# Performance work log

Measured on AMD Instinct MI355X. Metric: run time of the kernel, lower is better.

Reference implementation:

```python
import jax, jax.numpy as jnp
import numpy as np

EPS = 1e-7      # GENConv message epsilon
BN_EPS = 1e-5   # torch BatchNorm1d eps


def _genconv(x, src, dst, n, w1, b1, gamma, beta, w2, b2):
    # GENConv(aggr='softmax_sg', t=1.0): msg = relu(x_j)+eps, per-feature
    # scatter-softmax weights (stop-grad), weighted sum, residual, MLP
    # [Linear -> BatchNorm(train stats) -> ReLU -> Linear].
    msg = jnp.maximum(x[src], 0.0) + EPS                         # [E, d]
    m = jax.ops.segment_max(msg, dst, num_segments=n)            # [N, d]
    e = jnp.exp(msg - m[dst])
    s = jax.ops.segment_sum(e, dst, num_segments=n)
    alpha = jax.lax.stop_gradient(e / (s[dst] + 1e-16))          # softmax_sg
    agg = jax.ops.segment_sum(msg * alpha, dst, num_segments=n)  # [N, d]
    h = agg + x
    h = h @ w1 + b1
    mu = jnp.mean(h, axis=0)
    var = jnp.var(h, axis=0)
    h = (h - mu) * jax.lax.rsqrt(var + BN_EPS) * gamma + beta
    h = jnp.maximum(h, 0.0)
    return h @ w2 + b2


def _forward(x, edge_index, batch, target,
             g1_w1, g1_b1, g1_g, g1_be, g1_w2, g1_b2,
             g2_w1, g2_b1, g2_g, g2_be, g2_w2, g2_b2,
             g3_w1, g3_b1, g3_g, g3_be, g3_w2, g3_b2,
             fg1_w, fg1_b, fg2_w, fg2_b, fg3_w, fg3_b,
             emb, cw, cb, fxt_w, fxt_b,
             f1_w, f1_b, f2_w, f2_b, o_w, o_b):
    n = x.shape[0]
    nb = target.shape[0]
    src, dst = edge_index[0], edge_index[1]
    h = jnp.maximum(_genconv(x, src, dst, n, g1_w1, g1_b1, g1_g, g1_be, g1_w2, g1_b2), 0.0)
    h = jnp.maximum(_genconv(h, src, dst, n, g2_w1, g2_b1, g2_g, g2_be, g2_w2, g2_b2), 0.0)
    h = jnp.maximum(_genconv(h, src, dst, n, g3_w1, g3_b1, g3_g, g3_be, g3_w2, g3_b2), 0.0)
    # global mean pool over graphs
    sums = jax.ops.segment_sum(h, batch, num_segments=nb)
    cnt = jax.ops.segment_sum(jnp.ones((n, 1), h.dtype), batch, num_segments=nb)
    xg = sums / jnp.maximum(cnt, 1.0)
    xg = jnp.maximum(xg @ fg1_w + fg1_b, 0.0)
    xg = jnp.maximum(xg @ fg2_w + fg2_b, 0.0)
    xg = jnp.maximum(xg @ fg3_w + fg3_b, 0.0)
    # protein branch: embed [B,1000,128], Conv1d(1000->32,k=8) over embed axis
    ext = emb[target]                                            # [B, 1000, 128]
    conv = jax.lax.conv_general_dilated(
        ext, cw, (1,), 'VALID',
        dimension_numbers=('NCW', 'OIW', 'NCW')) + cb[None, :, None]  # [B, 32, 121]
    xt = conv.reshape(nb, 32 * 121) @ fxt_w + fxt_b
    xc = jnp.concatenate([xg, xt], axis=1)                       # [B, 256]
    xc = jnp.maximum(xc @ f1_w + f1_b, 0.0)
    xc = jnp.maximum(xc @ f2_w + f2_b, 0.0)
    return xc @ o_w + o_b


def _lin(k, i, o):
    kw, kb = jax.random.split(k)
    s = 1.0 / np.sqrt(i)
    return (jax.random.uniform(kw, (i, o), jnp.float32, -s, s),
            jax.random.uniform(kb, (o,), jnp.float32, -s, s))


def setup_inputs():
    key = jax.random.key(0)
    ks = jax.random.split(key, 32)
    N, E, B, D = 30000, 150000, 256, 78
    d = {}
    d['x'] = jax.random.normal(ks[0], (N, D), jnp.float32)
    d['edge_index'] = jax.random.randint(ks[1], (2, E), 0, N)
    d['batch'] = jnp.sort(jax.random.randint(ks[2], (N,), 0, B))
    d['target'] = jax.random.randint(ks[3], (B, 1000), 0, 26)
    dims = [(78, 156, 78), (78, 156, 312), (312, 624, 624)]
    for li, (i, hdim, o) in enumerate(dims, start=1):
        w1, b1 = _lin(ks[4 + 2 * li], i, hdim)
        w2, b2 = _lin(ks[5 + 2 * li], hdim, o)
        d['g%d_w1' % li], d['g%d_b1' % li] = w1, b1
        d['g%d_g' % li] = jnp.ones((hdim,), jnp.float32)
        d['g%d_be' % li] = jnp.zeros((hdim,), jnp.float32)
        d['g%d_w2' % li], d['g%d_b2' % li] = w2, b2
    d['fg1_w'], d['fg1_b'] = _lin(ks[14], 624, 512)
    d['fg2_w'], d['fg2_b'] = _lin(ks[15], 512, 1024)
    d['fg3_w'], d['fg3_b'] = _lin(ks[16], 1024, 128)
    d['emb'] = jax.random.normal(ks[17], (26, 128), jnp.float32)
    s = 1.0 / np.sqrt(1000 * 8)
    d['cw'] = jax.random.uniform(ks[18], (32, 1000, 8), jnp.float32, -s, s)
    d['cb'] = jax.random.uniform(ks[19], (32,), jnp.float32, -s, s)
    d['fxt_w'], d['fxt_b'] = _lin(ks[20], 32 * 121, 128)
    d['f1_w'], d['f1_b'] = _lin(ks[21], 256, 1024)
    d['f2_w'], d['f2_b'] = _lin(ks[22], 1024, 512)
    d['o_w'], d['o_b'] = _lin(ks[23], 512, 1)
    return d


def reference(x, edge_index, batch, target,
              g1_w1, g1_b1, g1_g, g1_be, g1_w2, g1_b2,
              g2_w1, g2_b1, g2_g, g2_be, g2_w2, g2_b2,
              g3_w1, g3_b1, g3_g, g3_be, g3_w2, g3_b2,
              fg1_w, fg1_b, fg2_w, fg2_b, fg3_w, fg3_b,
              emb, cw, cb, fxt_w, fxt_b,
              f1_w, f1_b, f2_w, f2_b, o_w, o_b):
    return _forward(x, edge_index, batch, target,
                    g1_w1, g1_b1, g1_g, g1_be, g1_w2, g1_b2,
                    g2_w1, g2_b1, g2_g, g2_be, g2_w2, g2_b2,
                    g3_w1, g3_b1, g3_g, g3_be, g3_w2, g3_b2,
                    fg1_w, fg1_b, fg2_w, fg2_b, fg3_w, fg3_b,
                    emb, cw, cb, fxt_w, fxt_b,
                    f1_w, f1_b, f2_w, f2_b, o_w, o_b)
```

## Files before the change

kernel.cpp:

```cpp
#include <hip/hip_runtime.h>
#include <hip/hip_bf16.h>

typedef unsigned short u16;
typedef __attribute__((ext_vector_type(8))) short bh8;
typedef __attribute__((ext_vector_type(4))) float f32x4;

static __device__ __forceinline__ float b2fu(u16 u) {
    union { float f; unsigned int i; } x;
    x.i = ((unsigned int)u) << 16;
    return x.f;
}
static __device__ __forceinline__ u16 f2bu(float f) {
    __hip_bfloat16 h = __float2bfloat16(f);
    union { __hip_bfloat16 h; u16 u; } x;
    x.h = h;
    return x.u;
}
static __device__ __forceinline__ void load2(const float* p, float& v0, float& v1) {
    float2 v = *reinterpret_cast<const float2*>(p);
    v0 = v.x; v1 = v.y;
}
static __device__ __forceinline__ void load2(const u16* p, float& v0, float& v1) {
    unsigned int u = *reinterpret_cast<const unsigned int*>(p);
    v0 = b2fu((u16)(u & 0xffff)); v1 = b2fu((u16)(u >> 16));
}

static __device__ __forceinline__ void gload16(const u16* g, u16* l) {
    __builtin_amdgcn_global_load_lds(
        (const __attribute__((address_space(1))) unsigned int*)(const void*)g,
        (__attribute__((address_space(3))) unsigned int*)(void*)l, 16, 0, 0);
}


__global__ __launch_bounds__(256) void const_out_kernel(float* __restrict__ out, float v, int n) {
    int i = blockIdx.x * 256 + threadIdx.x;
    if (i < n) out[i] = v;
}


__global__ __launch_bounds__(256) void hist_kernel(const int* __restrict__ dst,
                                                   int* __restrict__ hist, int E) {
    int e = blockIdx.x * 256 + threadIdx.x;
    if (e < E) atomicAdd(&hist[dst[e]], 1);
}

__global__ __launch_bounds__(256) void scan_kernel(const int* __restrict__ hist,
                                                   int* __restrict__ rowptr,
                                                   int* __restrict__ fill, int N) {
    __shared__ int csum[256];
    __shared__ int coff[257];
    int t = threadIdx.x;
    int chunk = (N + 255) / 256;
    int lo = min(t * chunk, N), hi = min(lo + chunk, N);
    int s = 0;
    for (int i = lo; i < hi; i++) s += hist[i];
    csum[t] = s;
    __syncthreads();
    if (t == 0) {
        int acc = 0;
        for (int i = 0; i < 256; i++) { coff[i] = acc; acc += csum[i]; }
        rowptr[N] = acc;
    }
    __syncthreads();
    int run = coff[t];
    for (int i = lo; i < hi; i++) {
        rowptr[i] = run;
        fill[i] = run;
        run += hist[i];
    }
}

__global__ __launch_bounds__(256) void scan_tiles(const int* __restrict__ hist, int N,
                                                  int* __restrict__ rowptr,
                                                  int* __restrict__ tsum) {
    int tid = threadIdx.x;
    int i = blockIdx.x * 256 + tid;
    int v = (i < N) ? hist[i] : 0;
    __shared__ int s[256];
    s[tid] = v;
    __syncthreads();
    for (int off = 1; off < 256; off <<= 1) {
        int t = (tid >= off) ? s[tid - off] : 0;
        __syncthreads();
        s[tid] += t;
        __syncthreads();
    }
    if (i < N) rowptr[i] = s[tid] - v;
    if (tid == 255) tsum[blockIdx.x] = s[255];
}

__global__ __launch_bounds__(256) void scan_tsum(const int* __restrict__ tsum, int ntiles,
                                                 int* __restrict__ toff,
                                                 int* __restrict__ totalp) {
    int tid = threadIdx.x;
    int v = (tid < ntiles) ? tsum[tid] : 0;
    __shared__ int s[256];
    s[tid] = v;
    __syncthreads();
    for (int off = 1; off < 256; off <<= 1) {
        int t = (tid >= off) ? s[tid - off] : 0;
        __syncthreads();
        s[tid] += t;
        __syncthreads();
    }
    if (tid < ntiles) toff[tid] = s[tid] - v;
    if (tid == 255) *totalp = s[255];
}

__global__ __launch_bounds__(256) void scan_apply(int* __restrict__ rowptr,
                                                  const int* __restrict__ toff, int N,
                                                  int* __restrict__ fill) {
    int i = blockIdx.x * 256 + threadIdx.x;
    if (i < N) {
        int r = rowptr[i] + toff[blockIdx.x];
        rowptr[i] = r;
        fill[i] = r;
    }
}

__global__ __launch_bounds__(256) void scatter_kernel(const int* __restrict__ src,
                                                      const int* __restrict__ dst,
                                                      int* __restrict__ fill,
                                                      int* __restrict__ srcs, int E) {
    int e = blockIdx.x * 256 + threadIdx.x;
    if (e < E) {
        int p = atomicAdd(&fill[dst[e]], 1);
        srcs[p] = src[e];
    }
}


template <typename T>
__global__ __launch_bounds__(256) void agg_kernel(const T* __restrict__ x,
                                                  const int* __restrict__ rowptr,
                                                  const int* __restrict__ srcs,
                                                  u16* __restrict__ out, int d, int Kp, int N) {
    int n = blockIdx.y * 4 + (threadIdx.x >> 6);
    int f = (blockIdx.x * 64 + (threadIdx.x & 63)) * 2;
    if (n >= N || f >= Kp) return;
    size_t o = (size_t)n * Kp + f;
    if (f >= d) {
        *reinterpret_cast<unsigned int*>(out + o) = 0;
        return;
    }
    int e0 = rowptr[n], e1 = rowptr[n + 1];
    float s0 = 0.f, t0 = 0.f, s1 = 0.f, t1 = 0.f;
    for (int e = e0; e < e1; e++) {
        int sr = srcs[e];
        float v0, v1;
        load2(x + (size_t)sr * d + f, v0, v1);
        float m0 = fmaxf(v0, 0.f) + 1e-7f;
        float w0 = __expf(m0);
        s0 += w0; t0 += m0 * w0;
        float m1 = fmaxf(v1, 0.f) + 1e-7f;
        float w1 = __expf(m1);
        s1 += w1; t1 += m1 * w1;
    }
    float x0, x1;
    load2(x + (size_t)n * d + f, x0, x1);
    float a0 = t0 / (s0 + 1e-16f) + x0;
    float a1 = t1 / (s1 + 1e-16f) + x1;
    unsigned int pk = (unsigned int)f2bu(a0) | ((unsigned int)f2bu(a1) << 16);
    *reinterpret_cast<unsigned int*>(out + o) = pk;
}


__global__ __launch_bounds__(256) void wt_cvt(const float* __restrict__ W, int K, int N,
                                              u16* __restrict__ WT, int Kp, int Np) {
    int n = blockIdx.y * 4 + (threadIdx.x >> 6);
    int k = blockIdx.x * 64 + (threadIdx.x & 63);
    if (n >= Np || k >= Kp) return;
    float v = (n < N && k < K) ? W[(size_t)k * N + n] : 0.f;
    WT[(size_t)n * Kp + k] = f2bu(v);
}


template <int AMODE, int EMODE, bool RELU, typename CT>
__global__ __launch_bounds__(256) void gemm_mfma(const u16* __restrict__ A,
                                                 const u16* __restrict__ BT,
                                                 const float* __restrict__ bias,
                                                 CT* __restrict__ C, int ldc, int M, int Ncols,
                                                 int Kp, int nbx, int nby, int spx,
                                                 const float* __restrict__ scale,
                                                 const float* __restrict__ shift,
                                                 float* __restrict__ osum,
                                                 float* __restrict__ osumsq) {
    int xcd = blockIdx.x & 7;
    int j = blockIdx.x >> 3;
    int bx = j % nbx;
    int by = xcd * spx + j / nbx;
    if (by >= nby) return;
    __shared__ u16 As[2][128 * 32];
    __shared__ u16 Bs[2][128 * 32];
    const int tid = threadIdx.x;
    const int lane = tid & 63;
    const int w = tid >> 6;
    const int bm = by * 128;
    const int bn = bx * 128;
    f32x4 acc[4][4] = {};

    const int r0 = w * 16 + (lane >> 2);
    const int r1 = r0 + 64;
    const int sw = ((lane & 3) ^ ((r0 >> 1) & 3)) << 3;
    const u16* Ag0 = A + (size_t)(bm + r0) * Kp + sw;
    const u16* Ag1 = A + (size_t)(bm + r1) * Kp + sw;
    const u16* Bg0 = BT + (size_t)(bn + r0) * Kp + sw;
    const u16* Bg1 = BT + (size_t)(bn + r1) * Kp + sw;
    const int wb = w << 9;

    uint4 a0r, a1r;
    auto stageB = [&](int b, int koff) {
        gload16(Bg0 + koff, &Bs[b][wb]);
        gload16(Bg1 + koff, &Bs[b][2048 + wb]);
    };
    auto stageA_lds = [&](int b, int koff) {
        gload16(Ag0 + koff, &As[b][wb]);
        gload16(Ag1 + koff, &As[b][2048 + wb]);
    };
    auto loadA_reg = [&](int koff) {
        a0r = *reinterpret_cast<const uint4*>(Ag0 + koff);
        a1r = *reinterpret_cast<const uint4*>(Ag1 + koff);
    };
    auto writeA_reg = [&](int b, int koff) {
        int f0 = sw + koff;
        float4 sc0 = *reinterpret_cast<const float4*>(scale + f0);
        float4 sc1 = *reinterpret_cast<const float4*>(scale + f0 + 4);
        float4 sh0 = *reinterpret_cast<const float4*>(shift + f0);
        float4 sh1 = *reinterpret_cast<const float4*>(shift + f0 + 4);
        auto tf2 = [](unsigned int u, float sa, float sb, float ha, float hb) {
            float h0 = b2fu((u16)(u & 0xffff)), h1 = b2fu((u16)(u >> 16));
            float v0 = fmaxf(fmaf(h0, sa, ha), 0.f);
            float v1 = fmaxf(fmaf(h1, sb, hb), 0.f);
            return (unsigned int)f2bu(v0) | ((unsigned int)f2bu(v1) << 16);
        };
        uint4 o0, o1;
        o0.x = tf2(a0r.x, sc0.x, sc0.y, sh0.x, sh0.y);
        o0.y = tf2(a0r.y, sc0.z, sc0.w, sh0.z, sh0.w);
        o0.z = tf2(a0r.z, sc1.x, sc1.y, sh1.x, sh1.y);
        o0.w = tf2(a0r.w, sc1.z, sc1.w, sh1.z, sh1.w);
        o1.x = tf2(a1r.x, sc0.x, sc0.y, sh0.x, sh0.y);
        o1.y = tf2(a1r.y, sc0.z, sc0.w, sh0.z, sh0.w);
        o1.z = tf2(a1r.z, sc1.x, sc1.y, sh1.x, sh1.y);
        o1.w = tf2(a1r.w, sc1.z, sc1.w, sh1.z, sh1.w);
        *reinterpret_cast<uint4*>(&As[b][wb + lane * 8]) = o0;
        *reinterpret_cast<uint4*>(&As[b][2048 + wb + lane * 8]) = o1;
    };

    const int fm = (w >> 1) * 64 + (lane & 15);
    const int fn = (w & 1) * 64 + (lane & 15);
    const int g = lane >> 4;
    const int ka = (g ^ ((fm >> 1) & 3)) << 3;
    const int kb = (g ^ ((fn >> 1) & 3)) << 3;

    const int nk = Kp >> 5;
    if constexpr (AMODE == 0) {
        stageA_lds(0, 0);
        stageB(0, 0);
        asm volatile("s_waitcnt vmcnt(0)" ::: "memory");
    } else {
        loadA_reg(0);
        stageB(0, 0);
        asm volatile("s_waitcnt vmcnt(0)" ::: "memory");
        writeA_reg(0, 0);
        asm volatile("s_waitcnt lgkmcnt(0)" ::: "memory");
    }
    __builtin_amdgcn_s_barrier();
    for (int k = 0; k < nk; k++) {
        const int cur = k & 1;
        if (k + 1 < nk) {
            if constexpr (AMODE == 0) stageA_lds(cur ^ 1, (k + 1) << 5);
            else loadA_reg((k + 1) << 5);
            stageB(cur ^ 1, (k + 1) << 5);
        }
        bh8 af[4], bf[4];
#pragma unroll
        for (int mt = 0; mt < 4; mt++)
            af[mt] = *reinterpret_cast<const bh8*>(&As[cur][(fm + mt * 16) * 32 + ka]);
#pragma unroll
        for (int nt = 0; nt < 4; nt++)
            bf[nt] = *reinterpret_cast<const bh8*>(&Bs[cur][(fn + nt * 16) * 32 + kb]);
        asm volatile("s_waitcnt lgkmcnt(0)" ::: "memory");
        __builtin_amdgcn_sched_barrier(0);
        __builtin_amdgcn_s_setprio(1);
#pragma unroll
        for (int mt = 0; mt < 4; mt++)
#pragma unroll
            for (int nt = 0; nt < 4; nt++)
                acc[mt][nt] = __builtin_amdgcn_mfma_f32_16x16x32_bf16(af[mt], bf[nt],
                                                                      acc[mt][nt], 0, 0, 0);
        __builtin_amdgcn_s_setprio(0);
        __builtin_amdgcn_sched_barrier(0);
        asm volatile("s_waitcnt vmcnt(0)" ::: "memory");
        if constexpr (AMODE == 1) {
            __builtin_amdgcn_sched_barrier(0);
            if (k + 1 < nk) writeA_reg(cur ^ 1, (k + 1) << 5);
            asm volatile("s_waitcnt lgkmcnt(0)" ::: "memory");
        }
        __builtin_amdgcn_s_barrier();
    }
    const int rq = (lane >> 4) * 4;
    const int cl = lane & 15;
    if constexpr (EMODE == 0) {
#pragma unroll
        for (int mt = 0; mt < 4; mt++) {
#pragma unroll
            for (int nt = 0; nt < 4; nt++) {
                int n = bn + (w & 1) * 64 + nt * 16 + cl;
                if (n >= Ncols) continue;
                float bv = bias[n];
#pragma unroll
                for (int r = 0; r < 4; r++) {
                    int m = bm + (w >> 1) * 64 + mt * 16 + rq + r;
                    if (m >= M) continue;
                    float v = acc[mt][nt][r] + bv;
                    if (RELU) v = fmaxf(v, 0.f);
                    if (sizeof(CT) == 2)
                        C[(size_t)m * ldc + n] = (CT)f2bu(v);
                    else
                        C[(size_t)m * ldc + n] = (CT)v;
                }
            }
        }
    } else {
        float cs[4] = {0.f, 0.f, 0.f, 0.f}, cq[4] = {0.f, 0.f, 0.f, 0.f};
#pragma unroll
        for (int nt = 0; nt < 4; nt++) {
            int n = bn + (w & 1) * 64 + nt * 16 + cl;
            if (n >= ldc) continue;
            float bv = (n < Ncols) ? bias[n] : 0.f;
#pragma unroll
            for (int mt = 0; mt < 4; mt++) {
#pragma unroll
                for (int r = 0; r < 4; r++) {
                    int m = bm + (w >> 1) * 64 + mt * 16 + rq + r;
                    if (m >= M) continue;
                    float v = (n < Ncols) ? acc[mt][nt][r] + bv : 0.f;
                    u16 vb = f2bu(v);
                    C[(size_t)m * ldc + n] = (CT)vb;
                    float vf = b2fu(vb);
                    cs[nt] += vf;
                    cq[nt] += vf * vf;
                }
            }
        }
        float* red = (float*)&As[0][0];
        const int slot = (w >> 1) * 4 + (lane >> 4);
#pragma unroll
        for (int nt = 0; nt < 4; nt++) {
            int nl = (w & 1) * 64 + nt * 16 + cl;
            red[nl * 8 + slot] = cs[nt];
            red[1024 + nl * 8 + slot] = cq[nt];
        }
        __syncthreads();
        if (tid < 128) {
            int n = bn + tid;
            if (n < Ncols) {
                float s = 0.f, q = 0.f;
#pragma unroll
                for (int i = 0; i < 8; i++) {
                    s += red[tid * 8 + i];
                    q += red[1024 + tid * 8 + i];
                }
                atomicAdd(&osum[n], s);
                atomicAdd(&osumsq[n], q);
            }
        }
    }
}


__global__ __launch_bounds__(256) void bn_final(const float* __restrict__ sum,
                                                const float* __restrict__ sumsq,
                                                const float* __restrict__ gamma,
                                                const float* __restrict__ beta,
                                                float* __restrict__ scale,
                                                float* __restrict__ shift, int dh, int Kp,
                                                float invN) {
    int i = blockIdx.x * 256 + threadIdx.x;
    if (i >= Kp) return;
    if (i < dh) {
        float mu = sum[i] * invN;
        float var = sumsq[i] * invN - mu * mu;
        float sc = gamma[i] / sqrtf(var + 1e-5f);
        scale[i] = sc;
        shift[i] = beta[i] - mu * sc;
    } else {
        scale[i] = 0.f;
        shift[i] = 0.f;
    }
}


__global__ __launch_bounds__(256) void pool_seg(const u16* __restrict__ h,
                                                const int* __restrict__ goff,
                                                float* __restrict__ gsum, int d) {
    int g = blockIdx.y;
    int c = threadIdx.x & 63;
    int f = blockIdx.x * 64 + c;
    int wv = threadIdx.x >> 6;
    int r0 = goff[g], r1 = goff[g + 1];
    float s = 0.f;
    if (f < d)
        for (int r = r0 + wv; r < r1; r += 4) s += b2fu(h[(size_t)r * d + f]);
    __shared__ float ls[4][64];
    ls[wv][c] = s;
    __syncthreads();
    if (wv == 0 && f < d) {
        float tot = ls[0][c] + ls[1][c] + ls[2][c] + ls[3][c];
        gsum[(size_t)g * d + f] = tot / fmaxf((float)(r1 - r0), 1.f);
    }
}


__global__ __launch_bounds__(256) void gemm_sk(const float* __restrict__ A, int lda,
                                               const float* __restrict__ B, int ldb,
                                               float* __restrict__ C, int ldc, int M, int K,
                                               int Nn, int KC) {
    __shared__ float As[16][17];
    __shared__ float Bs[16][68];
    const int tid = threadIdx.x;
    const int bn = blockIdx.x * 64;
    const int bm = blockIdx.y * 16;
    const int k0 = blockIdx.z * KC;
    const int kend = min(K, k0 + KC);
    const int tx = tid & 63;
    const int ty = tid >> 6;
    float acc[4] = {};
    const int am = bm + (tid >> 4);
    const int ak = tid & 15;
    for (int kk0 = k0; kk0 < kend; kk0 += 16) {
        {
            int k = kk0 + ak;
            As[ak][tid >> 4] = (am < M && k < kend) ? A[(size_t)am * lda + k] : 0.f;
        }
#pragma unroll
        for (int i = 0; i < 4; i++) {
            int k = kk0 + ty + 4 * i;
            Bs[ty + 4 * i][tx] = (k < kend && bn + tx < Nn) ? B[(size_t)k * ldb + bn + tx] : 0.f;
        }
        __syncthreads();
#pragma unroll
        for (int kk = 0; kk < 16; kk++) {
            float b = Bs[kk][tx];
#pragma unroll
            for (int i = 0; i < 4; i++) acc[i] = fmaf(As[kk][ty + 4 * i], b, acc[i]);
        }
        __syncthreads();
    }
    if (bn + tx < Nn) {
#pragma unroll
        for (int i = 0; i < 4; i++) {
            int m = bm + ty + 4 * i;
            if (m < M) atomicAdd(&C[(size_t)m * ldc + bn + tx], acc[i]);
        }
    }
}

__global__ __launch_bounds__(256) void bias_act(float* __restrict__ C, int ldc,
                                                const float* __restrict__ bias, int M, int Nn,
                                                int relu) {
    int idx = blockIdx.x * 256 + threadIdx.x;
    if (idx >= M * Nn) return;
    int m = idx / Nn, n = idx - m * Nn;
    float v = C[(size_t)m * ldc + n] + bias[n];
    C[(size_t)m * ldc + n] = relu ? fmaxf(v, 0.f) : v;
}

static void launch_gemm_small(const float* A, int lda, const float* B, int ldb,
                              const float* bias, float* C, int ldc, int M, int K, int Nn,
                              bool relu, hipStream_t stream) {
    int gx = (Nn + 63) / 64, gy = (M + 15) / 16;
    int tiles = gx * gy;
    int ksplit = 512 / tiles;
    if (ksplit < 1) ksplit = 1;
    int maxsplit = (K + 63) / 64;
    if (ksplit > maxsplit) ksplit = maxsplit;
    int KC = (((K + ksplit - 1) / ksplit) + 15) & ~15;
    ksplit = (K + KC - 1) / KC;
    gemm_sk<<<dim3(gx, gy, ksplit), 256, 0, stream>>>(A, lda, B, ldb, C, ldc, M, K, Nn, KC);
    bias_act<<<(M * Nn + 255) / 256, 256, 0, stream>>>(C, ldc, bias, M, Nn, relu ? 1 : 0);
}


__global__ __launch_bounds__(256) void hone_kernel(const int* __restrict__ target,
                                                   u16* __restrict__ H, int total) {
    int i = blockIdx.x * 256 + threadIdx.x;
    if (i >= total) return;
    int b = i / 1000, pos = i - b * 1000;
    int t = target[i];
    H[((size_t)b * 26 + t) * 1024 + pos] = 0x3F80;
}

__global__ __launch_bounds__(256) void cwt_cvt(const float* __restrict__ cw,
                                               u16* __restrict__ BT) {
    int n = blockIdx.y;
    int kk = blockIdx.x * 256 + threadIdx.x;
    int o = n >> 3, k = n & 7;
    float v = (kk < 1000) ? cw[(size_t)o * 8000 + (size_t)kk * 8 + k] : 0.f;
    BT[(size_t)n * 1024 + kk] = f2bu(v);
}

__global__ __launch_bounds__(256) void prot_conv_kernel(const float* __restrict__ S,
                                                        const float* __restrict__ emb,
                                                        const float* __restrict__ cb,
                                                        float* __restrict__ out) {
    int b = blockIdx.x;
    int tid = threadIdx.x;
    __shared__ float Sl[6656];
    __shared__ float el[26 * 128];
    for (int i = tid; i < 6656; i += 256) Sl[i] = S[(size_t)b * 6656 + i];
    for (int i = tid; i < 26 * 128; i += 256) el[i] = emb[i];
    __syncthreads();
    for (int j = tid; j < 3872; j += 256) {
        int o = j / 121;
        int w = j - o * 121;
        float acc = cb[o];
        for (int t = 0; t < 26; t++) {
#pragma unroll
            for (int k = 0; k < 8; k++)
                acc = fmaf(Sl[t * 256 + o * 8 + k], el[t * 128 + w + k], acc);
        }
        out[(size_t)b * 3872 + j] = acc;
    }
}


__global__ __launch_bounds__(256) void out_kernel(const float* __restrict__ A,
                                                  const float* __restrict__ w,
                                                  const float* __restrict__ bias,
                                                  float* __restrict__ out, int M, int K) {
    int wave = threadIdx.x >> 6;
    int lane = threadIdx.x & 63;
    int r = blockIdx.x * 4 + wave;
    if (r >= M) return;
    float acc = 0.f;
    for (int k = lane; k < K; k += 64) acc += A[(size_t)r * K + k] * w[k];
    for (int off = 32; off > 0; off >>= 1) acc += __shfl_down(acc, off, 64);
    if (lane == 0) out[r] = acc + bias[0];
}


static inline int KP(int k) { return (k + 31) & ~31; }
static inline int NP(int n) { return (n + 127) & ~127; }

extern "C" void kernel_launch(void* const* d_in, const int* in_sizes, int n_in, void* d_out,
                              int out_size, void* d_ws, size_t ws_size, hipStream_t stream) {
    static const int exp_sizes[39] = {
        2340000, 300000, 30000, 256000,
        12168, 156, 156, 156, 12168, 78,
        12168, 156, 156, 156, 48672, 312,
        194688, 624, 624, 624, 389376, 624,
        319488, 512, 524288, 1024, 131072, 128,
        3328, 256000, 32, 495616, 128,
        262144, 1024, 524288, 512, 512, 1};
    int bad = (n_in != 39) ? 100 : -1;
    if (bad < 0)
        for (int i = 0; i < 39; i++)
            if (in_sizes[i] != exp_sizes[i]) { bad = i; break; }
    if (bad >= 0) {
        const_out_kernel<<<1, 256, 0, stream>>>((float*)d_out, 2048.f + 8.f * bad, out_size);
        return;
    }

    const int N = 30000, E = 150000, B = 256;
    const int Mp = 30080;
    const int nby = 235, spx = 30;
    const int ntiles = (N + 255) / 256;
    const float* x_in = (const float*)d_in[0];
    const int* ei = (const int*)d_in[1];
    const int* src = ei;
    const int* dst = ei + E;
    const int* batch = (const int*)d_in[2];
    const int* target = (const int*)d_in[3];

    char* p = (char*)d_ws;
    auto carve = [&](size_t bytes) {
        char* r = p;
        p += (bytes + 15) & ~(size_t)15;
        return r;
    };
    int* hist = (int*)carve((size_t)(N + B) * 4);
    int* ghist = hist + N;
    int* rowptr = (int*)carve((size_t)(N + 1) * 4);
    int* fill = (int*)carve((size_t)N * 4);
    int* srcs = (int*)carve((size_t)E * 4);
    int* goff = (int*)carve((size_t)(B + 1) * 4);
    int* gfill = (int*)carve((size_t)B * 4);
    int* tsum = (int*)carve(256 * 4);
    int* toff = (int*)carve(256 * 4);
    float* sum_ = (float*)carve(2 * 624 * 4);
    float* sumsq_ = sum_ + 624;
    float* scale_ = (float*)carve(640 * 4);
    float* shift_ = (float*)carve(640 * 4);
    float* zero256 = (float*)carve(256 * 4);
    float* gsum = (float*)carve((size_t)B * 624 * 4);
    float* fc1 = (float*)carve((size_t)B * 512 * 4);
    float* fc2 = (float*)carve((size_t)B * 1024 * 4);
    float* xc = (float*)carve((size_t)B * 256 * 4);
    float* fcc1 = (float*)carve((size_t)B * 1024 * 4);
    float* fcc2 = (float*)carve((size_t)B * 512 * 4);
    float* Sbuf = (float*)carve((size_t)B * 6656 * 4);
    float* convb = (float*)carve((size_t)B * 3872 * 4);
    u16* Hbuf = (u16*)carve((size_t)B * 26 * 1024 * 2);
    u16* cwT = (u16*)carve((size_t)256 * 1024 * 2);
    u16* Abf = (u16*)carve((size_t)Mp * 640 * 2);
    u16* hmidb = (u16*)carve((size_t)Mp * 640 * 2);
    u16* Lout = (u16*)carve((size_t)N * 624 * 2);
    struct Layer { int di, dh, dn, w1, b1, g, be, w2, b2; };
    const Layer L[3] = {
        {78, 156, 78, 4, 5, 6, 7, 8, 9},
        {78, 156, 312, 10, 11, 12, 13, 14, 15},
        {312, 624, 624, 16, 17, 18, 19, 20, 21},
    };
    u16* WT1[3];
    u16* WT2[3];
    for (int li = 0; li < 3; li++) {
        WT1[li] = (u16*)carve((size_t)NP(L[li].dh) * KP(L[li].di) * 2);
        WT2[li] = (u16*)carve((size_t)NP(L[li].dn) * KP(L[li].dh) * 2);
    }
    size_t need = (size_t)(p - (char*)d_ws);
    if (ws_size < need) {
        const_out_kernel<<<1, 256, 0, stream>>>((float*)d_out,
                                                1024.f + (float)(ws_size >> 20), out_size);
        return;
    }

    hipMemsetAsync(hist, 0, (size_t)(N + B) * 4, stream);
    hipMemsetAsync(zero256, 0, 256 * 4, stream);
    hist_kernel<<<(E + 255) / 256, 256, 0, stream>>>(dst, hist, E);
    hist_kernel<<<(N + 255) / 256, 256, 0, stream>>>(batch, ghist, N);
    scan_tiles<<<ntiles, 256, 0, stream>>>(hist, N, rowptr, tsum);
    scan_tsum<<<1, 256, 0, stream>>>(tsum, ntiles, toff, rowptr + N);
    scan_apply<<<ntiles, 256, 0, stream>>>(rowptr, toff, N, fill);
    scan_kernel<<<1, 256, 0, stream>>>(ghist, goff, gfill, B);
    scatter_kernel<<<(E + 255) / 256, 256, 0, stream>>>(src, dst, fill, srcs, E);

    for (int li = 0; li < 3; li++) {
        int Kp1 = KP(L[li].di), Np1 = NP(L[li].dh);
        int Kp2 = KP(L[li].dh), Np2 = NP(L[li].dn);
        wt_cvt<<<dim3((Kp1 + 63) / 64, Np1 / 4), 256, 0, stream>>>(
            (const float*)d_in[L[li].w1], L[li].di, L[li].dh, WT1[li], Kp1, Np1);
        wt_cvt<<<dim3((Kp2 + 63) / 64, Np2 / 4), 256, 0, stream>>>(
            (const float*)d_in[L[li].w2], L[li].dh, L[li].dn, WT2[li], Kp2, Np2);
    }

    for (int li = 0; li < 3; li++) {
        const int di = L[li].di, dh = L[li].dh, dn = L[li].dn;
        const int Kp1 = KP(di), Kp2 = KP(dh);
        if (li == 0)
            agg_kernel<float><<<dim3((Kp1 / 2 + 63) / 64, (N + 3) / 4), 256, 0, stream>>>(
                x_in, rowptr, srcs, Abf, di, Kp1, N);
        else
            agg_kernel<u16><<<dim3((Kp1 / 2 + 63) / 64, (N + 3) / 4), 256, 0, stream>>>(
                Lout, rowptr, srcs, Abf, di, Kp1, N);
        hipMemsetAsync(sum_, 0, 2 * 624 * 4, stream);
        {
            int nbx = NP(dh) / 128;
            gemm_mfma<0, 1, false, u16><<<dim3(8 * spx * nbx), 256, 0, stream>>>(
                Abf, WT1[li], (const float*)d_in[L[li].b1], hmidb, Kp2, N, dh, Kp1, nbx, nby,
                spx, nullptr, nullptr, sum_, sumsq_);
        }
        bn_final<<<(Kp2 + 255) / 256, 256, 0, stream>>>(
            sum_, sumsq_, (const float*)d_in[L[li].g], (const float*)d_in[L[li].be], scale_,
            shift_, dh, Kp2, 1.0f / N);
        {
            int nbx = NP(dn) / 128;
            gemm_mfma<1, 0, true, u16><<<dim3(8 * spx * nbx), 256, 0, stream>>>(
                hmidb, WT2[li], (const float*)d_in[L[li].b2], Lout, dn, N, dn, Kp2, nbx, nby,
                spx, scale_, shift_, nullptr, nullptr);
        }
    }

    pool_seg<<<dim3(10, B), 256, 0, stream>>>(Lout, goff, gsum, 624);

    hipMemsetAsync(fc1, 0, (size_t)B * 3328 * 4, stream);

    launch_gemm_small(gsum, 624, (const float*)d_in[22], 512, (const float*)d_in[23], fc1, 512,
                      B, 624, 512, true, stream);
    launch_gemm_small(fc1, 512, (const float*)d_in[24], 1024, (const float*)d_in[25], fc2, 1024,
                      B, 512, 1024, true, stream);
    launch_gemm_small(fc2, 1024, (const float*)d_in[26], 128, (const float*)d_in[27], xc, 256,
                      B, 1024, 128, true, stream);

    hipMemsetAsync(Hbuf, 0, (size_t)B * 26 * 1024 * 2, stream);
    hone_kernel<<<(B * 1000 + 255) / 256, 256, 0, stream>>>(target, Hbuf, B * 1000);
    cwt_cvt<<<dim3(4, 256), 256, 0, stream>>>((const float*)d_in[29], cwT);
    {
        int nbxS = 2, nbyS = 52, spxS = 7;
        gemm_mfma<0, 0, false, float><<<dim3(8 * spxS * nbxS), 256, 0, stream>>>(
            Hbuf, cwT, zero256, Sbuf, 256, 6656, 256, 1024, nbxS, nbyS, spxS, nullptr, nullptr,
            nullptr, nullptr);
    }
    prot_conv_kernel<<<B, 256, 0, stream>>>(Sbuf, (const float*)d_in[28],
                                            (const float*)d_in[30], convb);
    launch_gemm_small(convb, 3872, (const float*)d_in[31], 128, (const float*)d_in[32],
                      xc + 128, 256, B, 3872, 128, false, stream);

    launch_gemm_small(xc, 256, (const float*)d_in[33], 1024, (const float*)d_in[34], fcc1, 1024,
                      B, 256, 1024, true, stream);
    launch_gemm_small(fcc1, 1024, (const float*)d_in[35], 512, (const float*)d_in[36], fcc2, 512,
                      B, 1024, 512, true, stream);
    out_kernel<<<(B + 3) / 4, 256, 0, stream>>>(fcc2, (const float*)d_in[37],
                                                (const float*)d_in[38], (float*)d_out, B, 512);
}
```

Measured before the change: 798.8 us.

## Split-K the protein conv GEMM, batch weight conversions, simplify BN stat accumulation

The protein-branch GEMM (K=1024) is split four ways across blockIdx.y and accumulates into a zeroed fp32 output with atomics. This raises parallelism on a grid that was otherwise small. In exchange it adds a memset of the output and atomic traffic, and makes float summation order nondeterministic. The six per-layer weight conversion launches are merged into one 3D-grid launch, and the BN statistics now sum the fp32 values rather than the bf16-rounded ones, which drops one conversion per element.

```diff
diff --git a/kernel.cpp b/kernel.cpp
--- a/kernel.cpp
+++ b/kernel.cpp
@@ -165,13 +165,21 @@
 }
 
 
-__global__ __launch_bounds__(256) void wt_cvt(const float* __restrict__ W, int K, int N,
-                                              u16* __restrict__ WT, int Kp, int Np) {
+struct WtJobs {
+    const float* W[6];
+    u16* WT[6];
+    int K[6], N[6], Kp[6], Np[6];
+};
+
+__global__ __launch_bounds__(256) void wt_cvt6(WtJobs jb) {
+    int jz = blockIdx.z;
+    int Kp = jb.Kp[jz], Np = jb.Np[jz];
     int n = blockIdx.y * 4 + (threadIdx.x >> 6);
     int k = blockIdx.x * 64 + (threadIdx.x & 63);
     if (n >= Np || k >= Kp) return;
-    float v = (n < N && k < K) ? W[(size_t)k * N + n] : 0.f;
-    WT[(size_t)n * Kp + k] = f2bu(v);
+    int K = jb.K[jz], N = jb.N[jz];
+    float v = (n < N && k < K) ? jb.W[jz][(size_t)k * N + n] : 0.f;
+    jb.WT[jz][(size_t)n * Kp + k] = f2bu(v);
 }
 
 
@@ -180,7 +188,7 @@
                                                  const u16* __restrict__ BT,
                                                  const float* __restrict__ bias,
                                                  CT* __restrict__ C, int ldc, int M, int Ncols,
-                                                 int Kp, int nbx, int nby, int spx,
+                                                 int Kp, int kLen, int nbx, int nby, int spx,
                                                  const float* __restrict__ scale,
                                                  const float* __restrict__ shift,
                                                  float* __restrict__ osum,
@@ -197,15 +205,16 @@
     const int w = tid >> 6;
     const int bm = by * 128;
     const int bn = bx * 128;
+    const int kw = blockIdx.y * kLen;
     f32x4 acc[4][4] = {};
 
     const int r0 = w * 16 + (lane >> 2);
     const int r1 = r0 + 64;
     const int sw = ((lane & 3) ^ ((r0 >> 1) & 3)) << 3;
-    const u16* Ag0 = A + (size_t)(bm + r0) * Kp + sw;
-    const u16* Ag1 = A + (size_t)(bm + r1) * Kp + sw;
-    const u16* Bg0 = BT + (size_t)(bn + r0) * Kp + sw;
-    const u16* Bg1 = BT + (size_t)(bn + r1) * Kp + sw;
+    const u16* Ag0 = A + (size_t)(bm + r0) * Kp + sw + kw;
+    const u16* Ag1 = A + (size_t)(bm + r1) * Kp + sw + kw;
+    const u16* Bg0 = BT + (size_t)(bn + r0) * Kp + sw + kw;
+    const u16* Bg1 = BT + (size_t)(bn + r1) * Kp + sw + kw;
     const int wb = w << 9;
 
     uint4 a0r, a1r;
@@ -222,7 +231,7 @@
         a1r = *reinterpret_cast<const uint4*>(Ag1 + koff);
     };
     auto writeA_reg = [&](int b, int koff) {
-        int f0 = sw + koff;
+        int f0 = sw + kw + koff;
         float4 sc0 = *reinterpret_cast<const float4*>(scale + f0);
         float4 sc1 = *reinterpret_cast<const float4*>(scale + f0 + 4);
         float4 sh0 = *reinterpret_cast<const float4*>(shift + f0);
@@ -252,7 +261,7 @@
     const int ka = (g ^ ((fm >> 1) & 3)) << 3;
     const int kb = (g ^ ((fn >> 1) & 3)) << 3;
 
-    const int nk = Kp >> 5;
+    const int nk = kLen >> 5;
     if constexpr (AMODE == 0) {
         stageA_lds(0, 0);
         stageB(0, 0);
@@ -321,7 +330,7 @@
                 }
             }
         }
-    } else {
+    } else if constexpr (EMODE == 1) {
         float cs[4] = {0.f, 0.f, 0.f, 0.f}, cq[4] = {0.f, 0.f, 0.f, 0.f};
 #pragma unroll
         for (int nt = 0; nt < 4; nt++) {
@@ -335,11 +344,9 @@
                     int m = bm + (w >> 1) * 64 + mt * 16 + rq + r;
                     if (m >= M) continue;
                     float v = (n < Ncols) ? acc[mt][nt][r] + bv : 0.f;
-                    u16 vb = f2bu(v);
-                    C[(size_t)m * ldc + n] = (CT)vb;
-                    float vf = b2fu(vb);
-                    cs[nt] += vf;
-                    cq[nt] += vf * vf;
+                    C[(size_t)m * ldc + n] = (CT)f2bu(v);
+                    cs[nt] += v;
+                    cq[nt] += v * v;
                 }
             }
         }
@@ -363,6 +370,21 @@
                 }
                 atomicAdd(&osum[n], s);
                 atomicAdd(&osumsq[n], q);
+            }
+        }
+    } else {
+#pragma unroll
+        for (int mt = 0; mt < 4; mt++) {
+#pragma unroll
+            for (int nt = 0; nt < 4; nt++) {
+                int n = bn + (w & 1) * 64 + nt * 16 + cl;
+                if (n >= Ncols) continue;
+#pragma unroll
+                for (int r = 0; r < 4; r++) {
+                    int m = bm + (w >> 1) * 64 + mt * 16 + rq + r;
+                    if (m >= M) continue;
+                    atomicAdd((float*)&C[(size_t)m * ldc + n], acc[mt][nt][r]);
+                }
             }
         }
     }
@@ -635,13 +657,25 @@
     scan_kernel<<<1, 256, 0, stream>>>(ghist, goff, gfill, B);
     scatter_kernel<<<(E + 255) / 256, 256, 0, stream>>>(src, dst, fill, srcs, E);
 
-    for (int li = 0; li < 3; li++) {
-        int Kp1 = KP(L[li].di), Np1 = NP(L[li].dh);
-        int Kp2 = KP(L[li].dh), Np2 = NP(L[li].dn);
-        wt_cvt<<<dim3((Kp1 + 63) / 64, Np1 / 4), 256, 0, stream>>>(
-            (const float*)d_in[L[li].w1], L[li].di, L[li].dh, WT1[li], Kp1, Np1);
-        wt_cvt<<<dim3((Kp2 + 63) / 64, Np2 / 4), 256, 0, stream>>>(
-            (const float*)d_in[L[li].w2], L[li].dh, L[li].dn, WT2[li], Kp2, Np2);
+    {
+        WtJobs jb;
+        int mgx = 1, mgy = 1;
+        for (int li = 0; li < 3; li++) {
+            jb.W[2 * li] = (const float*)d_in[L[li].w1];
+            jb.WT[2 * li] = WT1[li];
+            jb.K[2 * li] = L[li].di; jb.N[2 * li] = L[li].dh;
+            jb.Kp[2 * li] = KP(L[li].di); jb.Np[2 * li] = NP(L[li].dh);
+            jb.W[2 * li + 1] = (const float*)d_in[L[li].w2];
+            jb.WT[2 * li + 1] = WT2[li];
+            jb.K[2 * li + 1] = L[li].dh; jb.N[2 * li + 1] = L[li].dn;
+            jb.Kp[2 * li + 1] = KP(L[li].dh); jb.Np[2 * li + 1] = NP(L[li].dn);
+        }
+        for (int i = 0; i < 6; i++) {
+            int gx = (jb.Kp[i] + 63) / 64, gy = jb.Np[i] / 4;
+            if (gx > mgx) mgx = gx;
+            if (gy > mgy) mgy = gy;
+        }
+        wt_cvt6<<<dim3(mgx, mgy, 6), 256, 0, stream>>>(jb);
     }
 
     for (int li = 0; li < 3; li++) {
@@ -657,8 +691,8 @@
         {
             int nbx = NP(dh) / 128;
             gemm_mfma<0, 1, false, u16><<<dim3(8 * spx * nbx), 256, 0, stream>>>(
-                Abf, WT1[li], (const float*)d_in[L[li].b1], hmidb, Kp2, N, dh, Kp1, nbx, nby,
-                spx, nullptr, nullptr, sum_, sumsq_);
+                Abf, WT1[li], (const float*)d_in[L[li].b1], hmidb, Kp2, N, dh, Kp1, Kp1, nbx,
+                nby, spx, nullptr, nullptr, sum_, sumsq_);
         }
         bn_final<<<(Kp2 + 255) / 256, 256, 0, stream>>>(
             sum_, sumsq_, (const float*)d_in[L[li].g], (const float*)d_in[L[li].be], scale_,
@@ -666,8 +700,8 @@
         {
             int nbx = NP(dn) / 128;
             gemm_mfma<1, 0, true, u16><<<dim3(8 * spx * nbx), 256, 0, stream>>>(
-                hmidb, WT2[li], (const float*)d_in[L[li].b2], Lout, dn, N, dn, Kp2, nbx, nby,
-                spx, scale_, shift_, nullptr, nullptr);
+                hmidb, WT2[li], (const float*)d_in[L[li].b2], Lout, dn, N, dn, Kp2, Kp2, nbx,
+                nby, spx, scale_, shift_, nullptr, nullptr);
         }
     }
 
@@ -683,13 +717,14 @@
                       B, 1024, 128, true, stream);
 
     hipMemsetAsync(Hbuf, 0, (size_t)B * 26 * 1024 * 2, stream);
+    hipMemsetAsync(Sbuf, 0, (size_t)B * 6656 * 4, stream);
     hone_kernel<<<(B * 1000 + 255) / 256, 256, 0, stream>>>(target, Hbuf, B * 1000);
     cwt_cvt<<<dim3(4, 256), 256, 0, stream>>>((const float*)d_in[29], cwT);
     {
         int nbxS = 2, nbyS = 52, spxS = 7;
-        gemm_mfma<0, 0, false, float><<<dim3(8 * spxS * nbxS), 256, 0, stream>>>(
-            Hbuf, cwT, zero256, Sbuf, 256, 6656, 256, 1024, nbxS, nbyS, spxS, nullptr, nullptr,
-            nullptr, nullptr);
+        gemm_mfma<0, 2, false, float><<<dim3(8 * spxS * nbxS, 4), 256, 0, stream>>>(
+            Hbuf, cwT, zero256, Sbuf, 256, 6656, 256, 1024, 256, nbxS, nbyS, spxS, nullptr,
+            nullptr, nullptr, nullptr);
     }
     prot_conv_kernel<<<B, 256, 0, stream>>>(Sbuf, (const float*)d_in[28],
                                             (const float*)d_in[30], convb);
```

After: 808.9 us. About the same (+1.3%).
